# Kernel tuning notes

Measured on AMD Instinct MI355X. Metric: run time of the kernel, lower is better.

The kernel has to match this reference:

```python
import jax, jax.numpy as jnp
import numpy as np

NUM_HEADS = 16
HEAD_DIM = 64  # hidden_size 1024 / 16 heads


def setup_inputs() -> dict:
    key = jax.random.key(0)
    k1, k2, k3, k4 = jax.random.split(key, 4)
    B, S, H = 2, 2048, 1024
    qkv = jax.random.normal(k1, (B, S, H), dtype=jnp.float32)
    # True = masked position (tf.where(mask, -inf, scores))
    mask = jax.random.bernoulli(k2, 0.5, (B, S))
    Wqkv = jax.random.normal(k3, (H, 3 * H), dtype=jnp.float32) * (H ** -0.5)
    bqkv = jnp.zeros((3 * H,), dtype=jnp.float32)
    Wo = jax.random.normal(k4, (H, H), dtype=jnp.float32) * (H ** -0.5)
    bo = jnp.zeros((H,), dtype=jnp.float32)
    return {"qkv": qkv, "mask": mask, "Wqkv": Wqkv, "bqkv": bqkv, "Wo": Wo, "bo": bo}


def reference(qkv, mask, Wqkv, bqkv, Wo, bo):
    B, S, H = qkv.shape
    nh, hd = NUM_HEADS, HEAD_DIM
    proj = qkv @ Wqkv + bqkv                       # (B,S,3H)
    q, k, v = jnp.split(proj, 3, axis=-1)
    # NOTE: original MULTIPLIES query by sqrt(head_dim) (faithful to source)
    q = q * (hd ** 0.5)
    q = q.reshape(B, S, nh, hd).transpose(0, 2, 1, 3)   # (B,h,S,d)
    k = k.reshape(B, S, nh, hd).transpose(0, 2, 1, 3)
    v = v.reshape(B, S, nh, hd).transpose(0, 2, 1, 3)
    scores = jnp.einsum("bhqd,bhkd->bhqk", q, k)        # (B,h,S,S)
    scores = jnp.where(mask[:, None, None, :], -jnp.inf, scores)
    attn = jax.nn.softmax(scores, axis=-1)              # dropout identity at inference
    out = jnp.einsum("bhqk,bhkd->bhqd", attn, v)        # (B,h,S,d)
    out = out.transpose(0, 2, 1, 3).reshape(B, S, H)
    return out @ Wo + bo
```

## Files before the change

kernel.cpp:

```cpp
#include <hip/hip_runtime.h>

#define DEV __device__ __forceinline__

typedef unsigned short u16;
typedef unsigned int u32;
typedef __attribute__((ext_vector_type(4))) float f32x4;
typedef __attribute__((ext_vector_type(8))) short s16x8;
typedef __attribute__((ext_vector_type(8))) _Float16 f16x8;
typedef __attribute__((ext_vector_type(4))) unsigned short u16x4;
typedef __attribute__((ext_vector_type(4))) unsigned int u32x4;

#define BATCH 2
#define SEQ 2048
#define HID 1024
#define NH 16
#define HD 64

#define SCALE_XW 64.0f
#define INV_PROJ (1.0f / 4096.0f)
#define SCALE_Q 11.541560327111707f
#define SCALE_K 1.0f
#define DEFER_THR 10.0f

DEV f32x4 mfmah(s16x8 a, s16x8 b, f32x4 c) {
    return __builtin_amdgcn_mfma_f32_16x16x32_f16(
        __builtin_bit_cast(f16x8, a), __builtin_bit_cast(f16x8, b), c, 0, 0, 0);
}

DEV u16 f2h(float x) { return __builtin_bit_cast(u16, (_Float16)x); }
DEV float h2f(u16 h) { return (float)__builtin_bit_cast(_Float16, h); }

DEV u32 pkh(float a, float b) {
#if __has_builtin(__builtin_amdgcn_cvt_pkrtz)
    auto r = __builtin_amdgcn_cvt_pkrtz(a, b);
    return __builtin_bit_cast(u32, r);
#else
    return (u32)f2h(a) | ((u32)f2h(b) << 16);
#endif
}

DEV float fexp2(float x) {
#if __has_builtin(__builtin_amdgcn_exp2f)
    return __builtin_amdgcn_exp2f(x);
#else
    return exp2f(x);
#endif
}

DEV void swap32(int lane, u32 a, u32 b, u32& o0, u32& o1) {
#if __has_builtin(__builtin_amdgcn_permlane32_swap)
    auto r = __builtin_amdgcn_permlane32_swap((int)a, (int)b, false, false);
    o0 = (u32)r[0]; o1 = (u32)r[1];
#else
    u32 ax = (u32)__shfl_xor((int)a, 32);
    u32 bx = (u32)__shfl_xor((int)b, 32);
    bool hi = (lane & 32) != 0;
    o0 = hi ? bx : a;
    o1 = hi ? b : ax;
#endif
}
DEV void swap16(int lane, u32 a, u32 b, u32& o0, u32& o1) {
#if __has_builtin(__builtin_amdgcn_permlane16_swap)
    auto r = __builtin_amdgcn_permlane16_swap((int)a, (int)b, false, false);
    o0 = (u32)r[0]; o1 = (u32)r[1];
#else
    u32 ax = (u32)__shfl_xor((int)a, 16);
    u32 bx = (u32)__shfl_xor((int)b, 16);
    bool hi = (lane & 16) != 0;
    o0 = hi ? bx : a;
    o1 = hi ? b : ax;
#endif
}

DEV void gl_lds16(const void* g, void* l) {
    __builtin_amdgcn_global_load_lds(
        (__attribute__((address_space(1))) void*)(void*)g,
        (__attribute__((address_space(3))) void*)l, 16, 0, 0);
}

DEV void vm0_bar() {
    __builtin_amdgcn_sched_barrier(0);
    asm volatile("s_waitcnt vmcnt(0)" ::: "memory");
    __builtin_amdgcn_s_barrier();
    __builtin_amdgcn_sched_barrier(0);
}

DEV s16x8 lds_ld16(const u16* base, int row, int kbyte) {
    return *(const s16x8*)((const char*)base + row * 128 + (kbyte ^ ((row & 7) << 4)));
}
DEV s16x8 lds_ld16v(const u16* base, int row, int kbyte) {
    return *(const s16x8*)((const char*)base + row * 256 + (kbyte ^ ((row & 7) << 4)));
}
DEV s16x8 lds_ld32r(const u16* base, int row, int g) {
    return *(const s16x8*)((const char*)base + row * 64 + ((g * 16) ^ ((row & 3) << 4)));
}

__global__ __launch_bounds__(256) void prep_all(
    const float* __restrict__ qkv, const unsigned char* __restrict__ m,
    const float* __restrict__ Wqkv, const float* __restrict__ Wo,
    u16* __restrict__ Xh, u16* __restrict__ Wth, u16* __restrict__ Woth,
    float* __restrict__ pbias, int* __restrict__ pack_idx, int* __restrict__ cnt) {
    int bid = blockIdx.x;
    int tid = threadIdx.x;
    if (bid == 0) {
        __shared__ int sb, sf;
        __shared__ int scan[256];
        if (tid == 0) { sb = 0; sf = 0; }
        __syncthreads();
        int lb = 0, lf = 0;
        for (int i = tid * 16; i < tid * 16 + 16; i++) {
            unsigned char v = m[i];
            int pos = i & 3;
            if (pos == 3 && v == 0x3f) lf = 1;
            if (pos != 0 && v != 0) lb = 1;
        }
        if (lb) atomicOr(&sb, 1);
        if (lf) atomicOr(&sf, 1);
        __syncthreads();
        int f = sf ? 2 : (sb ? 1 : 0);
#pragma unroll
        for (int b = 0; b < BATCH; b++) {
            int base = b * SEQ;
            int keep[8], lc = 0;
#pragma unroll
            for (int e = 0; e < 8; e++) {
                int i = base + tid * 8 + e;
                int mv;
                if (f == 0) mv = ((const int*)m)[i] != 0;
                else if (f == 1) mv = m[i] != 0;
                else mv = ((const float*)m)[i] != 0.0f;
                keep[e] = !mv;
                lc += keep[e];
            }
            scan[tid] = lc;
            __syncthreads();
            for (int s = 1; s < 256; s <<= 1) {
                int v = (tid >= s) ? scan[tid - s] : 0;
                __syncthreads();
                scan[tid] += v;
                __syncthreads();
            }
            int off = scan[tid] - lc;
            int total = scan[255];
            __syncthreads();
#pragma unroll
            for (int e = 0; e < 8; e++)
                if (keep[e]) pack_idx[base + off++] = base + tid * 8 + e;
            if (tid == 0) cnt[b] = total;
            for (int j = tid; j < SEQ; j += 256)
                pbias[base + j] = (j < total) ? 0.0f : -1e30f;
        }
    } else if (bid <= 3072 + 1024) {
        const float* in;
        u16* oh;
        int N, t;
        float scale;
        if (bid <= 3072) { in = Wqkv; oh = Wth; N = 3072; t = bid - 1; scale = SCALE_XW; }
        else { in = Wo; oh = Woth; N = 1024; t = bid - 3073; scale = 1.0f; }
        const int K = 1024;
        int ntiles = N >> 5;
        int n0 = (t % ntiles) * 32, k0 = (t / ntiles) * 32;
        __shared__ float tt[32][33];
        int tx = tid & 31, ty = tid >> 5;
#pragma unroll
        for (int i = 0; i < 4; i++)
            tt[ty + 8 * i][tx] = in[(size_t)(k0 + ty + 8 * i) * N + n0 + tx];
        __syncthreads();
#pragma unroll
        for (int i = 0; i < 4; i++) {
            float v = tt[tx][ty + 8 * i] * scale;
            size_t o = (size_t)(n0 + ty + 8 * i) * K + k0 + tx;
            oh[o] = f2h(v);
        }
    } else {
        int cb = bid - 3073 - 1024;
#pragma unroll
        for (int it = 0; it < 4; it++) {
            int i = ((cb + it * 1024) * 256 + tid) * 4;
            f32x4 v = *(const f32x4*)&qkv[i];
            u16x4 h;
#pragma unroll
            for (int e = 0; e < 4; e++) h[e] = f2h(v[e] * SCALE_XW);
            *(u16x4*)&Xh[i] = h;
        }
    }
}

__global__ __launch_bounds__(256, 3) void gemm_qkv(
    const u16* __restrict__ Xh,
    const u16* __restrict__ Wth,
    const float* __restrict__ bqkv,
    const int* __restrict__ pack_idx, const int* __restrict__ cnt,
    u16* __restrict__ qh,
    u16* __restrict__ kh,
    u16* __restrict__ vt) {
    __shared__ __align__(16) u16 SM[2][128 * 64];
    int tid = threadIdx.x, lane = tid & 63, w = tid >> 6;
    int g = lane >> 4, q15 = lane & 15;
    int wm = w >> 1, wn = w & 1;
    int m0 = blockIdx.y * 128, n0 = blockIdx.x * 128;
    int part = n0 >> 10;
    int bb = m0 >> 11;
    int cb = cnt[bb];
    if (part != 0 && (m0 & 2047) >= cb) return;

    int srcrow[4];
#pragma unroll
    for (int i = 0; i < 4; i++) {
        int r = m0 + ((i * 256 + tid) >> 3);
        srcrow[i] = (part == 0) ? r : (((r & 2047) < cb) ? pack_idx[r] : (bb << 11));
    }

    f32x4 acc[4][4];
#pragma unroll
    for (int i = 0; i < 4; i++)
#pragma unroll
        for (int j = 0; j < 4; j++) acc[i][j] = (f32x4){0.f, 0.f, 0.f, 0.f};

    auto STAGE = [&](int kt) {
        int k0 = kt * 64;
#pragma unroll
        for (int i = 0; i < 4; i++) {
            int c = i * 256 + tid;
            int row = c >> 3, slot = c & 7;
            int sg = slot ^ (row & 7);
            int dst = (c & ~63) * 8;
            size_t ga = (size_t)srcrow[i] * 1024 + k0 + sg * 8;
            size_t gb = (size_t)(n0 + row) * 1024 + k0 + sg * 8;
            gl_lds16(&Xh[ga], &SM[0][dst]);
            gl_lds16(&Wth[gb], &SM[1][dst]);
        }
    };

    STAGE(0);
    for (int kt = 0; kt < 16; kt++) {
        vm0_bar();
        s16x8 a_h[2][4], b_h[2][4];
#pragma unroll
        for (int k2 = 0; k2 < 2; k2++) {
            int kb = k2 * 64 + g * 16;
#pragma unroll
            for (int i = 0; i < 4; i++) {
                a_h[k2][i] = lds_ld16(SM[0], wm * 64 + i * 16 + q15, kb);
                b_h[k2][i] = lds_ld16(SM[1], wn * 64 + i * 16 + q15, kb);
            }
        }
        __syncthreads();
        if (kt < 15) STAGE(kt + 1);
#pragma unroll
        for (int k2 = 0; k2 < 2; k2++)
#pragma unroll
            for (int mi = 0; mi < 4; mi++)
#pragma unroll
                for (int ni = 0; ni < 4; ni++)
                    acc[mi][ni] = mfmah(a_h[k2][mi], b_h[k2][ni], acc[mi][ni]);
    }

    if (part == 2) {
        u16* T = (u16*)SM;
        const int TP = 140;
#pragma unroll
        for (int h2 = 0; h2 < 2; h2++) {
            __syncthreads();
            if (wn == h2) {
#pragma unroll
                for (int mi = 0; mi < 4; mi++)
#pragma unroll
                    for (int ni = 0; ni < 4; ni++) {
                        int lcol = ni * 16 + q15;
#pragma unroll
                        for (int j = 0; j < 4; j++) {
                            int lrow = wm * 64 + mi * 16 + g * 4 + j;
                            T[lcol * TP + lrow] =
                                f2h(acc[mi][ni][j] * INV_PROJ + bqkv[n0 + h2 * 64 + lcol]);
                        }
                    }
            }
            __syncthreads();
            int lcol = tid >> 2;
            int seg = tid & 3;
            int c = n0 - 2048 + h2 * 64 + lcol;
            int h = c >> 6, d = c & 63;
            int b = m0 >> 11, sbase = m0 & 2047;
            size_t rowbase = ((size_t)(b * NH + h) * HD + d) * SEQ + sbase;
#pragma unroll
            for (int k = 0; k < 2; k++) {
                int slot = seg * 2 + k;
                *(s16x8*)&vt[rowbase + slot * 16 + 0] = *(const s16x8*)&T[lcol * TP + slot * 16 + 0];
                *(s16x8*)&vt[rowbase + slot * 16 + 8] = *(const s16x8*)&T[lcol * TP + slot * 16 + 8];
            }
        }
    } else {
#pragma unroll
        for (int mi = 0; mi < 4; mi++)
#pragma unroll
            for (int ni = 0; ni < 4; ni++) {
                int col = n0 + wn * 64 + ni * 16 + q15;
                float bias = bqkv[col];
                int cc = col & 1023, h = cc >> 6, d = cc & 63;
#pragma unroll
                for (int j = 0; j < 4; j++) {
                    int row = m0 + wm * 64 + mi * 16 + g * 4 + j;
                    int b = row >> 11, s = row & 2047;
                    float v = acc[mi][ni][j] * INV_PROJ + bias;
                    v *= (part == 0) ? SCALE_Q : SCALE_K;
                    size_t o = (size_t)(b * NH + h) * SEQ * HD + (size_t)s * HD + d;
                    if (part == 0) qh[o] = f2h(v);
                    else kh[o] = f2h(v);
                }
            }
    }
}

__global__ __launch_bounds__(512, 2) void attn_kernel(
    const u16* __restrict__ qh,
    const u16* __restrict__ kh,
    const u16* __restrict__ vt, const float* __restrict__ pbias,
    const int* __restrict__ cnt,
    u16* __restrict__ att) {
    __shared__ __align__(16) u16 Kh[2][8192], Vt[2][8192];
    __shared__ __align__(16) float MskB[2][128];
    int tid = threadIdx.x, lane = tid & 63, w = tid >> 6;
    int g = lane >> 4, q15 = lane & 15;
    int bid = blockIdx.y * 16 + blockIdx.x;
    int swz = (bid & 7) * 64 + (bid >> 3);
    int qt = swz & 15, bh = swz >> 4;
    int b = bh >> 4, h = bh & 15;
    int q0 = qt * 128;
    int NT = (cnt[b] + 127) >> 7;
    size_t base = (size_t)bh * SEQ * HD;
    const u16* vbase = vt + (size_t)bh * HD * SEQ;
    const float* mrow = pbias + b * SEQ;

    s16x8 aq[2];
#pragma unroll
    for (int k2 = 0; k2 < 2; k2++) {
        size_t o = base + (size_t)(q0 + w * 16 + q15) * HD + k2 * 32 + g * 8;
        aq[k2] = *(const s16x8*)&qh[o];
    }

    float m_ = -1e30f, l_ = 0.f;
    f32x4 o_[4];
#pragma unroll
    for (int df = 0; df < 4; df++) o_[df] = (f32x4){0.f, 0.f, 0.f, 0.f};

    auto STAGE = [&](int buf, int k0) {
#pragma unroll
        for (int i = 0; i < 2; i++) {
            int c = i * 512 + tid;
            int row = c >> 3, slot = c & 7;
            int sg = slot ^ (row & 7);
            int dst = (c & ~63) * 8;
            size_t gK = base + (size_t)(k0 + row) * HD + sg * 8;
            gl_lds16(&kh[gK], &Kh[buf][dst]);
            int vrow = c >> 4, vslot = c & 15;
            int vsg = vslot ^ (vrow & 7);
            size_t gV = (size_t)vrow * SEQ + k0 + vsg * 8;
            gl_lds16(&vbase[gV], &Vt[buf][dst]);
        }
        if (tid < 32) gl_lds16(&mrow[k0 + tid * 4], &MskB[buf][0]);
    };

    STAGE(0, 0);
    __syncthreads();

    for (int kt = 0; kt < NT; kt++) {
        int cur = kt & 1;
        if (kt < NT - 1) STAGE(cur ^ 1, (kt + 1) * 128);

        f32x4 sc[8];
#pragma unroll
        for (int nf = 0; nf < 8; nf++)
            sc[nf] = *(const f32x4*)&MskB[cur][nf * 16 + g * 4];
#pragma unroll
        for (int nf = 0; nf < 8; nf++)
#pragma unroll
            for (int k2 = 0; k2 < 2; k2++) {
                int kb = k2 * 64 + g * 16;
                s16x8 kbh = lds_ld16(Kh[cur], nf * 16 + q15, kb);
                sc[nf] = mfmah(kbh, aq[k2], sc[nf]);
            }

        float pml = -1e30f;
#pragma unroll
        for (int nf = 0; nf < 8; nf++) {
            float a = fmaxf(sc[nf][0], sc[nf][1]);
            float bmx = fmaxf(sc[nf][2], sc[nf][3]);
            pml = fmaxf(pml, fmaxf(a, bmx));
        }
        if (!__all(pml - m_ <= DEFER_THR)) {
            float pm = fmaxf(pml, __shfl_xor(pml, 16));
            pm = fmaxf(pm, __shfl_xor(pm, 32));
            float mn = fmaxf(m_, pm);
            float scl = fexp2(m_ - mn);
            m_ = mn;
            l_ *= scl;
#pragma unroll
            for (int j = 0; j < 4; j++) {
                float sb = __shfl(scl, g * 4 + j);
#pragma unroll
                for (int df = 0; df < 4; df++) o_[df][j] *= sb;
            }
        }
        float rs = 0.f;
        s16x8 pa[4];
#pragma unroll
        for (int k2 = 0; k2 < 4; k2++) {
            float p0[4], p1[4];
#pragma unroll
            for (int j = 0; j < 4; j++) {
                p0[j] = fexp2(sc[2 * k2][j] - m_);
                p1[j] = fexp2(sc[2 * k2 + 1][j] - m_);
                rs += p0[j] + p1[j];
            }
            u32 A0 = pkh(p0[0], p0[1]);
            u32 A1 = pkh(p0[2], p0[3]);
            u32 B0 = pkh(p1[0], p1[1]);
            u32 B1 = pkh(p1[2], p1[3]);
            u32 s0, s1, t0, t1, w0, w1, w2, w3;
            swap32(lane, A0, B0, s0, s1);
            swap16(lane, s0, s1, w0, w2);
            swap32(lane, A1, B1, t0, t1);
            swap16(lane, t0, t1, w1, w3);
            u32x4 words = {w0, w1, w2, w3};
            pa[k2] = __builtin_bit_cast(s16x8, words);
        }
        l_ += rs;

#pragma unroll
        for (int k2 = 0; k2 < 4; k2++) {
            int kb = k2 * 64 + g * 16;
#pragma unroll
            for (int df = 0; df < 4; df++) {
                s16x8 vb = lds_ld16v(Vt[cur], df * 16 + q15, kb);
                o_[df] = mfmah(pa[k2], vb, o_[df]);
            }
        }
        __syncthreads();
    }

    float lt = l_;
    lt += __shfl_xor(lt, 16);
    lt += __shfl_xor(lt, 32);
#pragma unroll
    for (int j = 0; j < 4; j++) {
        float lb = __shfl(lt, g * 4 + j);
        float linv = __builtin_amdgcn_rcpf(lb);
        int qrow = q0 + w * 16 + g * 4 + j;
        size_t srow = (size_t)(b * SEQ + qrow);
#pragma unroll
        for (int df = 0; df < 4; df++) {
            int col = h * HD + df * 16 + q15;
            att[srow * HID + col] = f2h(o_[df][j] * linv);
        }
    }
}

__global__ __launch_bounds__(256, 4) void gemm_out(
    const u16* __restrict__ A, const u16* __restrict__ Bh0,
    const float* __restrict__ bo, float* __restrict__ out) {
    __shared__ __align__(16) u16 SMa[2][64 * 32], SMb[2][128 * 32];
    int tid = threadIdx.x, lane = tid & 63, w = tid >> 6;
    int g = lane >> 4, q15 = lane & 15;
    int wm = w >> 1, wn = w & 1;
    int m0 = blockIdx.y * 64, n0 = blockIdx.x * 128;
    f32x4 acc[2][4];
#pragma unroll
    for (int i = 0; i < 2; i++)
#pragma unroll
        for (int j = 0; j < 4; j++) acc[i][j] = (f32x4){0.f, 0.f, 0.f, 0.f};

    auto STAGE = [&](int db, int kt) {
        int k0 = kt * 32;
        {
            int c = tid;
            int row = c >> 2, slot = c & 3;
            int sg = slot ^ (row & 3);
            int dst = (c & ~63) * 8;
            gl_lds16(&A[(size_t)(m0 + row) * 1024 + k0 + sg * 8], &SMa[db][dst]);
        }
#pragma unroll
        for (int i = 0; i < 2; i++) {
            int c = i * 256 + tid;
            int row = c >> 2, slot = c & 3;
            int sg = slot ^ (row & 3);
            int dst = (c & ~63) * 8;
            gl_lds16(&Bh0[(size_t)(n0 + row) * 1024 + k0 + sg * 8], &SMb[db][dst]);
        }
    };

    STAGE(0, 0);
    for (int kt = 0; kt < 32; kt++) {
        int cur = kt & 1;
        __syncthreads();
        if (kt < 31) STAGE(cur ^ 1, kt + 1);
        s16x8 a_[2], b_[4];
#pragma unroll
        for (int i = 0; i < 2; i++)
            a_[i] = lds_ld32r(SMa[cur], wm * 32 + i * 16 + q15, g);
#pragma unroll
        for (int i = 0; i < 4; i++)
            b_[i] = lds_ld32r(SMb[cur], wn * 64 + i * 16 + q15, g);
#pragma unroll
        for (int mi = 0; mi < 2; mi++)
#pragma unroll
            for (int ni = 0; ni < 4; ni++)
                acc[mi][ni] = mfmah(a_[mi], b_[ni], acc[mi][ni]);
    }
#pragma unroll
    for (int mi = 0; mi < 2; mi++)
#pragma unroll
        for (int ni = 0; ni < 4; ni++) {
            int col = n0 + wn * 64 + ni * 16 + q15;
            float bias = bo[col];
#pragma unroll
            for (int j = 0; j < 4; j++) {
                int row = m0 + wm * 32 + mi * 16 + g * 4 + j;
                out[(size_t)row * 1024 + col] = acc[mi][ni][j] + bias;
            }
        }
}

extern "C" void kernel_launch(void* const* d_in, const int* in_sizes, int n_in,
                              void* d_out, int out_size, void* d_ws, size_t ws_size,
                              hipStream_t stream) {
    const float* qkv = (const float*)d_in[0];
    const void* mask = d_in[1];
    const float* Wqkv = (const float*)d_in[2];
    const float* bqkv = (const float*)d_in[3];
    const float* Wo = (const float*)d_in[4];
    const float* bo = (const float*)d_in[5];
    float* out = (float*)d_out;

    const size_t SZ_X = (size_t)4096 * 1024 * 2;
    const size_t SZ_W = (size_t)3072 * 1024 * 2;
    const size_t SZ_WO = (size_t)1024 * 1024 * 2;
    const size_t SZ_QKV = (size_t)32 * 2048 * 64 * 2;
    const size_t SZ_ATT = (size_t)4096 * 1024 * 2;

    char* p = (char*)d_ws;
    u16* Xh = (u16*)p; p += SZ_X;
    u16* Wth = (u16*)p; p += SZ_W;
    u16* Woth = (u16*)p; p += SZ_WO;
    u16* qh = (u16*)p; p += SZ_QKV;
    u16* kh = (u16*)p; p += SZ_QKV;
    u16* vt = (u16*)p; p += SZ_QKV;
    u16* att = (u16*)p; p += SZ_ATT;
    float* pbias = (float*)p; p += BATCH * SEQ * 4;
    int* pack_idx = (int*)p; p += BATCH * SEQ * 4;
    int* cnt = (int*)p; p += 256;

    prep_all<<<1 + 3072 + 1024 + 1024, 256, 0, stream>>>(
        qkv, (const unsigned char*)mask, Wqkv, Wo, Xh, Wth, Woth, pbias, pack_idx, cnt);
    gemm_qkv<<<dim3(24, 32), 256, 0, stream>>>(Xh, Wth, bqkv, pack_idx, cnt, qh, kh, vt);
    attn_kernel<<<dim3(16, 32), 512, 0, stream>>>(qh, kh, vt, pbias, cnt, att);
    gemm_out<<<dim3(8, 64), 256, 0, stream>>>(att, Woth, bo, out);
}
```

Baseline: 97.16 us.

## Use single-buffered BK=64 LDS tiles with register prefetch in output GEMM

Rewrites the output-projection GEMM main loop to stage 64-wide K tiles in one LDS buffer instead of double-buffered 32-wide tiles. Each iteration loads all fragments into registers, syncs, issues the next tile's global->LDS copy, then runs the MFMAs, so the copy overlaps compute. This halves the number of barriers and loop iterations and uses 8-way XOR swizzled rows. In exchange, each iteration now also waits for its own load to complete and holds more live fragment registers.

```diff
diff --git a/kernel.cpp b/kernel.cpp
--- a/kernel.cpp
+++ b/kernel.cpp
@@ -90,9 +90,6 @@
 }
 DEV s16x8 lds_ld16v(const u16* base, int row, int kbyte) {
     return *(const s16x8*)((const char*)base + row * 256 + (kbyte ^ ((row & 7) << 4)));
-}
-DEV s16x8 lds_ld32r(const u16* base, int row, int g) {
-    return *(const s16x8*)((const char*)base + row * 64 + ((g * 16) ^ ((row & 3) << 4)));
 }
 
 __global__ __launch_bounds__(256) void prep_all(
@@ -459,7 +456,7 @@
 __global__ __launch_bounds__(256, 4) void gemm_out(
     const u16* __restrict__ A, const u16* __restrict__ Bh0,
     const float* __restrict__ bo, float* __restrict__ out) {
-    __shared__ __align__(16) u16 SMa[2][64 * 32], SMb[2][128 * 32];
+    __shared__ __align__(16) u16 SMa[64 * 64], SMb[128 * 64];
     int tid = threadIdx.x, lane = tid & 63, w = tid >> 6;
     int g = lane >> 4, q15 = lane & 15;
     int wm = w >> 1, wn = w & 1;
@@ -470,42 +467,49 @@
 #pragma unroll
         for (int j = 0; j < 4; j++) acc[i][j] = (f32x4){0.f, 0.f, 0.f, 0.f};
 
-    auto STAGE = [&](int db, int kt) {
-        int k0 = kt * 32;
-        {
-            int c = tid;
-            int row = c >> 2, slot = c & 3;
-            int sg = slot ^ (row & 3);
-            int dst = (c & ~63) * 8;
-            gl_lds16(&A[(size_t)(m0 + row) * 1024 + k0 + sg * 8], &SMa[db][dst]);
-        }
+    auto STAGE = [&](int kt) {
+        int k0 = kt * 64;
 #pragma unroll
         for (int i = 0; i < 2; i++) {
             int c = i * 256 + tid;
-            int row = c >> 2, slot = c & 3;
-            int sg = slot ^ (row & 3);
+            int row = c >> 3, slot = c & 7;
+            int sg = slot ^ (row & 7);
             int dst = (c & ~63) * 8;
-            gl_lds16(&Bh0[(size_t)(n0 + row) * 1024 + k0 + sg * 8], &SMb[db][dst]);
+            gl_lds16(&A[(size_t)(m0 + row) * 1024 + k0 + sg * 8], &SMa[dst]);
+        }
+#pragma unroll
+        for (int i = 0; i < 4; i++) {
+            int c = i * 256 + tid;
+            int row = c >> 3, slot = c & 7;
+            int sg = slot ^ (row & 7);
+            int dst = (c & ~63) * 8;
+            gl_lds16(&Bh0[(size_t)(n0 + row) * 1024 + k0 + sg * 8], &SMb[dst]);
         }
     };
 
-    STAGE(0, 0);
-    for (int kt = 0; kt < 32; kt++) {
-        int cur = kt & 1;
+    STAGE(0);
+    for (int kt = 0; kt < 16; kt++) {
+        vm0_bar();
+        s16x8 a_[2][2], b_[2][4];
+#pragma unroll
+        for (int k2 = 0; k2 < 2; k2++) {
+            int kb = k2 * 64 + g * 16;
+#pragma unroll
+            for (int i = 0; i < 2; i++)
+                a_[k2][i] = lds_ld16(SMa, wm * 32 + i * 16 + q15, kb);
+#pragma unroll
+            for (int i = 0; i < 4; i++)
+                b_[k2][i] = lds_ld16(SMb, wn * 64 + i * 16 + q15, kb);
+        }
         __syncthreads();
-        if (kt < 31) STAGE(cur ^ 1, kt + 1);
-        s16x8 a_[2], b_[4];
-#pragma unroll
-        for (int i = 0; i < 2; i++)
-            a_[i] = lds_ld32r(SMa[cur], wm * 32 + i * 16 + q15, g);
-#pragma unroll
-        for (int i = 0; i < 4; i++)
-            b_[i] = lds_ld32r(SMb[cur], wn * 64 + i * 16 + q15, g);
-#pragma unroll
-        for (int mi = 0; mi < 2; mi++)
-#pragma unroll
-            for (int ni = 0; ni < 4; ni++)
-                acc[mi][ni] = mfmah(a_[mi], b_[ni], acc[mi][ni]);
+        if (kt < 15) STAGE(kt + 1);
+#pragma unroll
+        for (int k2 = 0; k2 < 2; k2++)
+#pragma unroll
+            for (int mi = 0; mi < 2; mi++)
+#pragma unroll
+                for (int ni = 0; ni < 4; ni++)
+                    acc[mi][ni] = mfmah(a_[k2][mi], b_[k2][ni], acc[mi][ni]);
     }
 #pragma unroll
     for (int mi = 0; mi < 2; mi++)
```

After: 92.82 us. 1.05x faster.
